# Performance work log

Hardware: AMD Instinct MI355X
Metric: run time of the kernel (lower is better)

## Reference

```python
import jax, jax.numpy as jnp
import numpy as np

NUM_FEATURES = 5
MUL_FACTOR = 2.0


def setup_inputs() -> dict:
    key = jax.random.key(0)
    x = jax.random.normal(key, (4096, 512), dtype=jnp.float32)
    # buffer from __init__: mul_factor ** (arange(F) - F // 2)
    bandwidth_multipliers = (MUL_FACTOR ** (jnp.arange(NUM_FEATURES) - NUM_FEATURES // 2)).astype(jnp.float32)
    return {"x": x, "bandwidth_multipliers": bandwidth_multipliers}


def _cdist(x):
    # pairwise Euclidean distance, p=2
    sq = jnp.sum(x * x, axis=1)
    d2 = sq[:, None] + sq[None, :] - 2.0 * (x @ x.T)
    return jnp.sqrt(jnp.maximum(d2, 0.0))


def reference(x, bandwidth_multipliers):
    d = _cdist(x)  # [N, N]
    n = d.shape[0]
    # heuristic bandwidth on detached distances (self.bandwidth is None)
    bw = jax.lax.stop_gradient(d).sum() / (n * (n - 1))
    bws = bw * bandwidth_multipliers  # [F]
    # exp over F bandwidths, summed: [F, N, N] -> [N, N]
    return jnp.exp(-d[None, :, :] / bws[:, None, None]).sum(axis=0)
```

## Files before the change

kernel.cpp:

```cpp
#include <hip/hip_runtime.h>
#include <cstdint>
#include <cstddef>

#define N_PTS 4096
#define KDIM  512
#define NFEAT 5

typedef __attribute__((ext_vector_type(8))) short bf16x8;
typedef __attribute__((ext_vector_type(4))) float f32x4;
typedef uint32_t u32;

__device__ inline unsigned short f2bf(float f) {
  union { float f; u32 u; } v; v.f = f;
  u32 r = (v.u + 0x7fffu + ((v.u >> 16) & 1u)) >> 16;
  return (unsigned short)r;
}

__device__ inline void bf2f2(u32 u, float& a, float& b) {
  union { u32 u; float f; } x, y;
  x.u = u << 16; y.u = u & 0xffff0000u;
  a = x.f; b = y.f;
}

__device__ inline void load_lds16(const void* g, void* l) {
  __builtin_amdgcn_global_load_lds(
      (const __attribute__((address_space(1))) void*)g,
      (__attribute__((address_space(3))) void*)l, 16, 0, 0);
}

__global__ __launch_bounds__(256) void prep_kernel(const float* __restrict__ X,
                                                   short* __restrict__ Xb,
                                                   float* __restrict__ sq,
                                                   float* __restrict__ gsum) {
  if (blockIdx.x == 0 && threadIdx.x == 0) *gsum = 0.f;
  const int row = blockIdx.x;
  const int t = threadIdx.x;
  const float2 v = ((const float2*)(X + (size_t)row * KDIM))[t];
  short2 b;
  b.x = (short)f2bf(v.x);
  b.y = (short)f2bf(v.y);
  ((short2*)(Xb + (size_t)row * KDIM))[t] = b;
  float s = v.x * v.x + v.y * v.y;
#pragma unroll
  for (int off = 32; off; off >>= 1) s += __shfl_down(s, off);
  __shared__ float ws[4];
  if ((t & 63) == 0) ws[t >> 6] = s;
  __syncthreads();
  if (t == 0) sq[row] = ws[0] + ws[1] + ws[2] + ws[3];
}

__global__ __launch_bounds__(256, 3) void dist_kernel(
    const short* __restrict__ Xb, const float* __restrict__ sq,
    unsigned short* __restrict__ Dw, float* __restrict__ gsum) {
  __shared__ short As[128 * 64];
  __shared__ short Bs[128 * 64];
  __shared__ float red[4];

  const int tid = threadIdx.x;
  const int lane = tid & 63;
  const int wid = tid >> 6;
  const int wave_m = wid >> 1, wave_n = wid & 1;
  const int lhi = lane >> 4, llo = lane & 15;
  const int bm = blockIdx.y, bn = blockIdx.x;

  f32x4 acc[4][4];
#pragma unroll
  for (int i = 0; i < 4; ++i)
#pragma unroll
    for (int j = 0; j < 4; ++j) acc[i][j] = (f32x4){0.f, 0.f, 0.f, 0.f};

  const int srow = tid >> 3;
  const int sgran = (tid & 7) ^ (srow & 7);
  const size_t ga0 = (size_t)(bm * 128 + srow) * KDIM + sgran * 8;
  const size_t gb0 = (size_t)(bn * 128 + srow) * KDIM + sgran * 8;

  for (int kt = 0; kt < KDIM / 64; ++kt) {
    const int koff = kt * 64;
#pragma unroll
    for (int g = 0; g < 4; ++g) {
      load_lds16(Xb + ga0 + (size_t)g * 32 * KDIM + koff, (char*)As + g * 4096 + tid * 16);
      load_lds16(Xb + gb0 + (size_t)g * 32 * KDIM + koff, (char*)Bs + g * 4096 + tid * 16);
    }
    __syncthreads();

#pragma unroll
    for (int h = 0; h < 2; ++h) {
      bf16x8 a[4], b[4];
#pragma unroll
      for (int i = 0; i < 4; ++i) {
        const int ra = wave_m * 64 + i * 16 + llo;
        const int rb = wave_n * 64 + i * 16 + llo;
        const int c = h * 4 + lhi;
        a[i] = *(const bf16x8*)&As[ra * 64 + ((c ^ (ra & 7)) << 3)];
        b[i] = *(const bf16x8*)&Bs[rb * 64 + ((c ^ (rb & 7)) << 3)];
      }
#pragma unroll
      for (int i = 0; i < 4; ++i)
#pragma unroll
        for (int j = 0; j < 4; ++j)
          acc[i][j] =
              __builtin_amdgcn_mfma_f32_16x16x32_bf16(a[i], b[j], acc[i][j], 0, 0, 0);
    }
    __syncthreads();
  }

  float lsum = 0.f;
  const int gi0 = bm * 128, gj0 = bn * 128;
  const int r_base = wave_m * 64 + lhi * 4;
  const int c_base = wave_n * 64 + llo;
  float sqj[4];
#pragma unroll
  for (int j = 0; j < 4; ++j) sqj[j] = sq[gj0 + c_base + j * 16];

  const size_t tile_base =
      ((size_t)(bm * 32 + bn)) * 16384 + (size_t)wid * 4096;

#pragma unroll
  for (int i = 0; i < 4; ++i) {
    union { unsigned short s[16]; uint4 q[2]; } pk;
#pragma unroll
    for (int rr = 0; rr < 4; ++rr) {
      const int r = r_base + i * 16 + rr;
      const float sqi = sq[gi0 + r];
#pragma unroll
      for (int j = 0; j < 4; ++j) {
        const int c = c_base + j * 16;
        float d2 = sqi + sqj[j] - 2.f * acc[i][j][rr];
        float dd = sqrtf(fmaxf(d2, 0.f));
        if (gi0 + r == gj0 + c) dd = 0.f;
        lsum += dd;
        pk.s[rr * 4 + j] = f2bf(dd);
      }
    }
    unsigned short* dst = Dw + tile_base + (size_t)i * 1024;
    *(uint4*)(dst + lane * 8) = pk.q[0];
    *(uint4*)(dst + 512 + lane * 8) = pk.q[1];
  }

#pragma unroll
  for (int off = 32; off; off >>= 1) lsum += __shfl_down(lsum, off);
  if (lane == 0) red[wid] = lsum;
  __syncthreads();
  if (tid == 0) atomicAdd(gsum, red[0] + red[1] + red[2] + red[3]);
}

__global__ __launch_bounds__(256) void rbf_kernel(
    const unsigned short* __restrict__ Dw, const float* __restrict__ gsum,
    const float* __restrict__ mult, float* __restrict__ out) {
  const float bw = *gsum * (1.0f / ((float)N_PTS * (float)(N_PTS - 1)));
  float c[NFEAT];
#pragma unroll
  for (int f = 0; f < NFEAT; ++f) c[f] = -1.0f / (bw * mult[f]);

  const int b = blockIdx.x;
  const int bm = b >> 5, bn = b & 31;
  const int tid = threadIdx.x;
  const int lane = tid & 63;
  const int wid = tid >> 6;
  const int wave_m = wid >> 1, wave_n = wid & 1;
  const int lhi = lane >> 4, llo = lane & 15;

  const size_t tile_base = (size_t)b * 16384 + (size_t)wid * 4096;
  const int gi0 = bm * 128 + wave_m * 64 + lhi * 4;
  const int gj0 = bn * 128 + wave_n * 64 + llo;

#pragma unroll
  for (int i = 0; i < 4; ++i) {
    const unsigned short* src = Dw + tile_base + (size_t)i * 1024;
    const uint4 q0 = *(const uint4*)(src + lane * 8);
    const uint4 q1 = *(const uint4*)(src + 512 + lane * 8);
    float v[16];
    bf2f2(q0.x, v[0], v[1]);   bf2f2(q0.y, v[2], v[3]);
    bf2f2(q0.z, v[4], v[5]);   bf2f2(q0.w, v[6], v[7]);
    bf2f2(q1.x, v[8], v[9]);   bf2f2(q1.y, v[10], v[11]);
    bf2f2(q1.z, v[12], v[13]); bf2f2(q1.w, v[14], v[15]);

    float o[16];
#pragma unroll
    for (int e = 0; e < 16; ++e) {
      float a = 0.f;
#pragma unroll
      for (int f = 0; f < NFEAT; ++f) a += __expf(v[e] * c[f]);
      o[e] = a;
    }

#pragma unroll
    for (int rr = 0; rr < 4; ++rr) {
      float* orow = out + (size_t)(gi0 + i * 16 + rr) * N_PTS + gj0;
#pragma unroll
      for (int j = 0; j < 4; ++j) orow[j * 16] = o[rr * 4 + j];
    }
  }
}

extern "C" void kernel_launch(void* const* d_in, const int* in_sizes, int n_in,
                              void* d_out, int out_size, void* d_ws, size_t ws_size,
                              hipStream_t stream) {
  const float* X = (const float*)d_in[0];
  const float* mult = (const float*)d_in[1];
  float* out = (float*)d_out;

  char* ws = (char*)d_ws;
  float* gsum = (float*)ws;
  float* sq = (float*)(ws + 1024);
  short* Xb = (short*)(ws + 1024 + N_PTS * sizeof(float));
  unsigned short* Dw = (unsigned short*)(ws + 1024 + N_PTS * sizeof(float) +
                                         (size_t)N_PTS * KDIM * sizeof(short));

  prep_kernel<<<N_PTS, 256, 0, stream>>>(X, Xb, sq, gsum);
  dist_kernel<<<dim3(32, 32), 256, 0, stream>>>(Xb, sq, Dw, gsum);
  rbf_kernel<<<1024, 256, 0, stream>>>(Dw, gsum, mult, out);
}
```

Measured before the change: 126.8 us.

## Pre-swizzle bf16 X into MFMA fragment layout and load operands directly from global

The prep kernel now writes the bf16 copy of X in a layout that matches the MFMA 16x16x32 fragment order, and handles four rows per block with 16-byte vector loads. The GEMM kernel drops LDS staging and barriers entirely: each wave loads its A/B fragments straight from global memory with one-step register double-buffering. This removes LDS traffic and syncthreads, but each wave now fetches its operands independently, so reuse relies on L2 and global latency is only partly hidden by the prefetch.

```diff
diff --git a/kernel.cpp b/kernel.cpp
--- a/kernel.cpp
+++ b/kernel.cpp
@@ -22,40 +22,35 @@
   a = x.f; b = y.f;
 }
 
-__device__ inline void load_lds16(const void* g, void* l) {
-  __builtin_amdgcn_global_load_lds(
-      (const __attribute__((address_space(1))) void*)g,
-      (__attribute__((address_space(3))) void*)l, 16, 0, 0);
-}
-
 __global__ __launch_bounds__(256) void prep_kernel(const float* __restrict__ X,
-                                                   short* __restrict__ Xb,
+                                                   short* __restrict__ Xf,
                                                    float* __restrict__ sq,
                                                    float* __restrict__ gsum) {
-  if (blockIdx.x == 0 && threadIdx.x == 0) *gsum = 0.f;
-  const int row = blockIdx.x;
   const int t = threadIdx.x;
-  const float2 v = ((const float2*)(X + (size_t)row * KDIM))[t];
-  short2 b;
-  b.x = (short)f2bf(v.x);
-  b.y = (short)f2bf(v.y);
-  ((short2*)(Xb + (size_t)row * KDIM))[t] = b;
-  float s = v.x * v.x + v.y * v.y;
+  if (blockIdx.x == 0 && t == 0) *gsum = 0.f;
+  const int r = blockIdx.x * 4 + (t >> 6);
+  const int g = t & 63;
+  const float* src = X + (size_t)r * KDIM + g * 8;
+  const float4 u0 = ((const float4*)src)[0];
+  const float4 u1 = ((const float4*)src)[1];
+  union { unsigned short s[8]; uint4 q; } pk;
+  pk.s[0] = f2bf(u0.x); pk.s[1] = f2bf(u0.y);
+  pk.s[2] = f2bf(u0.z); pk.s[3] = f2bf(u0.w);
+  pk.s[4] = f2bf(u1.x); pk.s[5] = f2bf(u1.y);
+  pk.s[6] = f2bf(u1.z); pk.s[7] = f2bf(u1.w);
+  const int p = r >> 4, c = g >> 2, l = ((g & 3) << 4) | (r & 15);
+  *(uint4*)(Xf + (size_t)(p * 16 + c) * 512 + l * 8) = pk.q;
+  float s = u0.x * u0.x + u0.y * u0.y + u0.z * u0.z + u0.w * u0.w +
+            u1.x * u1.x + u1.y * u1.y + u1.z * u1.z + u1.w * u1.w;
 #pragma unroll
   for (int off = 32; off; off >>= 1) s += __shfl_down(s, off);
-  __shared__ float ws[4];
-  if ((t & 63) == 0) ws[t >> 6] = s;
-  __syncthreads();
-  if (t == 0) sq[row] = ws[0] + ws[1] + ws[2] + ws[3];
+  if (g == 0) sq[r] = s;
 }
 
 __global__ __launch_bounds__(256, 3) void dist_kernel(
-    const short* __restrict__ Xb, const float* __restrict__ sq,
+    const short* __restrict__ Xf, const float* __restrict__ sq,
     unsigned short* __restrict__ Dw, float* __restrict__ gsum) {
-  __shared__ short As[128 * 64];
-  __shared__ short Bs[128 * 64];
   __shared__ float red[4];
-
   const int tid = threadIdx.x;
   const int lane = tid & 63;
   const int wid = tid >> 6;
@@ -63,45 +58,42 @@
   const int lhi = lane >> 4, llo = lane & 15;
   const int bm = blockIdx.y, bn = blockIdx.x;
 
+  const short* baseA = Xf + (size_t)(bm * 8 + wave_m * 4) * 8192 + lane * 8;
+  const short* baseB = Xf + (size_t)(bn * 8 + wave_n * 4) * 8192 + lane * 8;
+
   f32x4 acc[4][4];
 #pragma unroll
   for (int i = 0; i < 4; ++i)
 #pragma unroll
     for (int j = 0; j < 4; ++j) acc[i][j] = (f32x4){0.f, 0.f, 0.f, 0.f};
 
-  const int srow = tid >> 3;
-  const int sgran = (tid & 7) ^ (srow & 7);
-  const size_t ga0 = (size_t)(bm * 128 + srow) * KDIM + sgran * 8;
-  const size_t gb0 = (size_t)(bn * 128 + srow) * KDIM + sgran * 8;
-
-  for (int kt = 0; kt < KDIM / 64; ++kt) {
-    const int koff = kt * 64;
-#pragma unroll
-    for (int g = 0; g < 4; ++g) {
-      load_lds16(Xb + ga0 + (size_t)g * 32 * KDIM + koff, (char*)As + g * 4096 + tid * 16);
-      load_lds16(Xb + gb0 + (size_t)g * 32 * KDIM + koff, (char*)Bs + g * 4096 + tid * 16);
-    }
-    __syncthreads();
-
-#pragma unroll
-    for (int h = 0; h < 2; ++h) {
-      bf16x8 a[4], b[4];
+  bf16x8 ca[4], cb[4];
+#pragma unroll
+  for (int i = 0; i < 4; ++i) {
+    ca[i] = *(const bf16x8*)(baseA + i * 8192);
+    cb[i] = *(const bf16x8*)(baseB + i * 8192);
+  }
+
+#pragma unroll
+  for (int c = 0; c < 16; ++c) {
+    bf16x8 na[4], nb[4];
+    if (c < 15) {
 #pragma unroll
       for (int i = 0; i < 4; ++i) {
-        const int ra = wave_m * 64 + i * 16 + llo;
-        const int rb = wave_n * 64 + i * 16 + llo;
-        const int c = h * 4 + lhi;
-        a[i] = *(const bf16x8*)&As[ra * 64 + ((c ^ (ra & 7)) << 3)];
-        b[i] = *(const bf16x8*)&Bs[rb * 64 + ((c ^ (rb & 7)) << 3)];
+        na[i] = *(const bf16x8*)(baseA + (c + 1) * 512 + i * 8192);
+        nb[i] = *(const bf16x8*)(baseB + (c + 1) * 512 + i * 8192);
       }
-#pragma unroll
-      for (int i = 0; i < 4; ++i)
-#pragma unroll
-        for (int j = 0; j < 4; ++j)
-          acc[i][j] =
-              __builtin_amdgcn_mfma_f32_16x16x32_bf16(a[i], b[j], acc[i][j], 0, 0, 0);
-    }
-    __syncthreads();
+    }
+#pragma unroll
+    for (int i = 0; i < 4; ++i)
+#pragma unroll
+      for (int j = 0; j < 4; ++j)
+        acc[i][j] =
+            __builtin_amdgcn_mfma_f32_16x16x32_bf16(ca[i], cb[j], acc[i][j], 0, 0, 0);
+    if (c < 15) {
+#pragma unroll
+      for (int i = 0; i < 4; ++i) { ca[i] = na[i]; cb[i] = nb[i]; }
+    }
   }
 
   float lsum = 0.f;
@@ -112,8 +104,7 @@
 #pragma unroll
   for (int j = 0; j < 4; ++j) sqj[j] = sq[gj0 + c_base + j * 16];
 
-  const size_t tile_base =
-      ((size_t)(bm * 32 + bn)) * 16384 + (size_t)wid * 4096;
+  const size_t tile_base = ((size_t)(bm * 32 + bn)) * 16384 + (size_t)wid * 4096;
 
 #pragma unroll
   for (int i = 0; i < 4; ++i) {
@@ -203,11 +194,11 @@
   char* ws = (char*)d_ws;
   float* gsum = (float*)ws;
   float* sq = (float*)(ws + 1024);
-  short* Xb = (short*)(ws + 1024 + N_PTS * sizeof(float));
+  short* Xf = (short*)(ws + 1024 + N_PTS * sizeof(float));
   unsigned short* Dw = (unsigned short*)(ws + 1024 + N_PTS * sizeof(float) +
                                          (size_t)N_PTS * KDIM * sizeof(short));
 
-  prep_kernel<<<N_PTS, 256, 0, stream>>>(X, Xb, sq, gsum);
-  dist_kernel<<<dim3(32, 32), 256, 0, stream>>>(Xb, sq, Dw, gsum);
+  prep_kernel<<<N_PTS / 4, 256, 0, stream>>>(X, Xf, sq, gsum);
+  dist_kernel<<<dim3(32, 32), 256, 0, stream>>>(Xf, sq, Dw, gsum);
   rbf_kernel<<<1024, 256, 0, stream>>>(Dw, gsum, mult, out);
 }
```

After: 137.4 us. +8.4%, slower.
